# Kernel tuning notes

Hardware: AMD Instinct MI355X
Metric: run time of the kernel (lower is better)

Reference implementation:

```python
import jax, jax.numpy as jnp
import numpy as np

EMB = 1024
HEADS = 16
HD = EMB // HEADS  # 64
FF = 4 * EMB
EPS = 1e-5


def _layernorm(x, g, b):
    mu = jnp.mean(x, axis=-1, keepdims=True)
    var = jnp.mean(jnp.square(x - mu), axis=-1, keepdims=True)
    return (x - mu) * jax.lax.rsqrt(var + EPS) * g + b


def setup_inputs() -> dict:
    key = jax.random.key(0)
    ks = jax.random.split(key, 12)
    s_in = 1.0 / np.sqrt(EMB)
    s_ff = 1.0 / np.sqrt(FF)
    return {
        "x": jax.random.normal(ks[0], (4, 2048, EMB), dtype=jnp.float32),
        # per-head projections stacked: [H, C, HD]
        "Wq": jax.random.normal(ks[1], (HEADS, EMB, HD), dtype=jnp.float32) * s_in,
        "Wk": jax.random.normal(ks[2], (HEADS, EMB, HD), dtype=jnp.float32) * s_in,
        "Wv": jax.random.normal(ks[3], (HEADS, EMB, HD), dtype=jnp.float32) * s_in,
        "Wo": jax.random.normal(ks[4], (EMB, EMB), dtype=jnp.float32) * s_in,
        "bo": jnp.zeros((EMB,), dtype=jnp.float32),
        "W1": jax.random.normal(ks[5], (EMB, FF), dtype=jnp.float32) * s_in,
        "b1": jnp.zeros((FF,), dtype=jnp.float32),
        "W2": jax.random.normal(ks[6], (FF, EMB), dtype=jnp.float32) * s_ff,
        "b2": jnp.zeros((EMB,), dtype=jnp.float32),
        "g1": jnp.ones((EMB,), dtype=jnp.float32),
        "be1": jnp.zeros((EMB,), dtype=jnp.float32),
        "g2": jnp.ones((EMB,), dtype=jnp.float32),
        "be2": jnp.zeros((EMB,), dtype=jnp.float32),
    }


def reference(x, Wq, Wk, Wv, Wo, bo, W1, b1, W2, b2, g1, be1, g2, be2):
    B, T, C = x.shape
    h = _layernorm(x, g1, be1)
    # per-head projections: [B,H,T,HD]
    q = jnp.einsum("btc,hcd->bhtd", h, Wq)
    k = jnp.einsum("btc,hcd->bhtd", h, Wk)
    v = jnp.einsum("btc,hcd->bhtd", h, Wv)
    scores = jnp.einsum("bhtd,bhsd->bhts", q, k) * (HD ** -0.5)
    causal = jnp.tril(jnp.ones((T, T), dtype=bool))
    scores = jnp.where(causal, scores, -jnp.inf)
    attn = jax.nn.softmax(scores, axis=-1)
    out = jnp.einsum("bhts,bhsd->bhtd", attn, v)
    out = out.transpose(0, 2, 1, 3).reshape(B, T, C)  # concat heads
    x = x + out @ Wo + bo
    h2 = _layernorm(x, g2, be2)
    x = x + jax.nn.relu(h2 @ W1 + b1) @ W2 + b2
    return x
```

## Files before the change

### kernel.cpp

```cpp
#include <hip/hip_runtime.h>

typedef unsigned short u16;
typedef unsigned int u32;
typedef float f32x4 __attribute__((ext_vector_type(4)));
typedef short s16x8 __attribute__((ext_vector_type(8)));
typedef u16 u16x4 __attribute__((ext_vector_type(4)));
typedef u32 u32x2 __attribute__((ext_vector_type(2)));
typedef u32 u32x4 __attribute__((ext_vector_type(4)));

#define DEVI static __device__ __forceinline__

DEVI u16 f2bf(float f) {
  u32 u = __float_as_uint(f);
  return (u16)((u + 0x7fffu + ((u >> 16) & 1u)) >> 16);
}

DEVI float fexp2(float x) {
#if __has_builtin(__builtin_amdgcn_exp2f)
  return __builtin_amdgcn_exp2f(x);
#else
  return __expf(x * 0.69314718056f);
#endif
}

DEVI void g2l16(const void* g, void* l) {
  __builtin_amdgcn_global_load_lds((const __attribute__((address_space(1))) u32*)g,
                                   (__attribute__((address_space(3))) u32*)l,
                                   16, 0, 0);
}

__global__ __launch_bounds__(256) void trans_w(
    const float* __restrict__ src, u16* __restrict__ dst, int R, int C)
{
  __shared__ __attribute__((aligned(16))) u16 tile[64 * 65];
  const int t = threadIdx.x;
  const int c0 = blockIdx.x * 64, r0 = blockIdx.y * 64;
#pragma unroll
  for (int i = 0; i < 16; ++i) {
    const int idx = i * 256 + t;
    const int c = idx & 63, r = idx >> 6;
    tile[c * 65 + r] = f2bf(src[(long)(r0 + r) * C + c0 + c]);
  }
  __syncthreads();
#pragma unroll
  for (int i = 0; i < 16; ++i) {
    const int idx = i * 256 + t;
    const int r = idx & 63, c = idx >> 6;
    dst[(long)(c0 + c) * R + r0 + r] = tile[c * 65 + r];
  }
}

__global__ __launch_bounds__(256) void trans_qkvw(
    const float* __restrict__ Wq, const float* __restrict__ Wk,
    const float* __restrict__ Wv, u16* __restrict__ dst)
{
  __shared__ __attribute__((aligned(16))) u16 tile[64 * 65];
  const int t = threadIdx.x;
  const int c0 = blockIdx.x * 64;
  const int mh = blockIdx.y;
  const int mat = mh >> 4, h = mh & 15;
  const float* src = (mat == 0 ? Wq : (mat == 1 ? Wk : Wv)) + (long)h * 65536;
#pragma unroll
  for (int i = 0; i < 16; ++i) {
    const int idx = i * 256 + t;
    const int d = idx & 63, c = idx >> 6;
    tile[d * 65 + c] = f2bf(src[(long)(c0 + c) * 64 + d]);
  }
  __syncthreads();
  const long nb = (long)(mat * 1024 + h * 64);
#pragma unroll
  for (int i = 0; i < 16; ++i) {
    const int idx = i * 256 + t;
    const int d = idx >> 6, c = idx & 63;
    dst[(nb + d) * 1024 + c0 + c] = tile[d * 65 + c];
  }
}

__global__ __launch_bounds__(256) void vtrans(
    const u16* __restrict__ qkv, u16* __restrict__ vtg)
{
  __shared__ __attribute__((aligned(16))) u32 tile[64 * 33];
  const int t = threadIdx.x;
  const int tt = blockIdx.x, bh = blockIdx.y;
  const long bt0 = (long)(bh >> 4) * 2048;
  const int h = bh & 15;
  const int t0 = tt * 64;
  const int r2 = t >> 3, c8 = t & 7;
  const u16* src = qkv + (bt0 + t0 + 2 * r2) * 3072 + 2048 + h * 64 + c8 * 8;
  const s16x8 a = *(const s16x8*)src;
  const s16x8 b = *(const s16x8*)(src + 3072);
#pragma unroll
  for (int j = 0; j < 8; ++j)
    tile[(c8 * 8 + j) * 33 + r2] = (u32)(u16)a[j] | ((u32)(u16)b[j] << 16);
  __syncthreads();
#pragma unroll
  for (int it = 0; it < 2; ++it) {
    const int idx = it * 256 + t;
    const int d = idx >> 3, g = idx & 7;
    u32 p0 = tile[d * 33 + g];
    u32 p1 = tile[d * 33 + g + 8];
    u32 p2 = tile[d * 33 + g + 16];
    u32 p3 = tile[d * 33 + g + 24];
    u32x4 w;
    w[0] = (p0 & 0xffffu) | (p1 << 16);
    w[1] = (p2 & 0xffffu) | (p3 << 16);
    w[2] = (p0 >> 16) | (p1 & 0xffff0000u);
    w[3] = (p2 >> 16) | (p3 & 0xffff0000u);
    *(u32x4*)(vtg + (long)bh * 131072 + (long)d * 2048 + t0 + g * 8) = w;
  }
}

__global__ __launch_bounds__(256) void ln_kernel(
    const float* __restrict__ x, const float* __restrict__ g,
    const float* __restrict__ be, u16* __restrict__ out)
{
  const int t = threadIdx.x, wv = t >> 6, l = t & 63;
  const long row = (long)blockIdx.x * 4 + wv;
  const float* xr = x + row * 1024;
  f32x4 v[4];
#pragma unroll
  for (int i = 0; i < 4; ++i) v[i] = *(const f32x4*)(xr + i * 256 + l * 4);
  float s = 0.f, sq = 0.f;
#pragma unroll
  for (int i = 0; i < 4; ++i)
#pragma unroll
    for (int j = 0; j < 4; ++j) { s += v[i][j]; sq += v[i][j] * v[i][j]; }
#pragma unroll
  for (int mask = 1; mask < 64; mask <<= 1) {
    s  += __shfl_xor(s, mask);
    sq += __shfl_xor(sq, mask);
  }
  const float mean = s * (1.f / 1024.f);
  const float var  = sq * (1.f / 1024.f) - mean * mean;
  const float rs = rsqrtf(var + 1e-5f);
#pragma unroll
  for (int i = 0; i < 4; ++i) {
    f32x4 gv = *(const f32x4*)(g  + i * 256 + l * 4);
    f32x4 bv = *(const f32x4*)(be + i * 256 + l * 4);
    u16x4 o;
#pragma unroll
    for (int j = 0; j < 4; ++j) o[j] = f2bf((v[i][j] - mean) * rs * gv[j] + bv[j]);
    *(u16x4*)(out + row * 1024 + i * 256 + l * 4) = o;
  }
}

template <typename OutT, bool RELU, bool BIAS, bool RESID>
__global__ __launch_bounds__(256) void gemm_bt(
    const u16* __restrict__ A, const u16* __restrict__ Bt,
    OutT* __restrict__ Cout, const float* __restrict__ bias,
    const float* __restrict__ resid, int M, int N, int K)
{
  __shared__ __attribute__((aligned(16))) u16 As[4096];
  __shared__ __attribute__((aligned(16))) u16 Bs[4096];
  const int t  = threadIdx.x;
  const int l  = t & 63;
  const int wv = t >> 6;
  const int lr = l & 15, lg = l >> 4;
  const int wr = wv >> 1, wc = wv & 1;
  const long m0 = (long)blockIdx.x * 128, n0 = (long)blockIdx.y * 128;

  const int srow = t >> 2;
  const int scol = (t & 3) << 3;

  f32x4 acc[4][4] = {};

  const u16* Ap = A  + (m0 + srow) * K + scol;
  const u16* Bp = Bt + (n0 + srow) * K + scol;
  char* Asd = (char*)As + t * 16;
  char* Bsd = (char*)Bs + t * 16;

  for (int k0 = 0; k0 < K; k0 += 32) {
    __syncthreads();
    g2l16(Ap + k0,                Asd);
    g2l16(Ap + (long)64 * K + k0, Asd + 4096);
    g2l16(Bp + k0,                Bsd);
    g2l16(Bp + (long)64 * K + k0, Bsd + 4096);
    __syncthreads();
    s16x8 af[4], bfr[4];
#pragma unroll
    for (int m = 0; m < 4; ++m)
      af[m] = *(const s16x8*)(As + (wr * 64 + m * 16 + lr) * 32 + lg * 8);
#pragma unroll
    for (int n = 0; n < 4; ++n)
      bfr[n] = *(const s16x8*)(Bs + (wc * 64 + n * 16 + lr) * 32 + lg * 8);
#pragma unroll
    for (int m = 0; m < 4; ++m)
#pragma unroll
      for (int n = 0; n < 4; ++n)
        acc[m][n] = __builtin_amdgcn_mfma_f32_16x16x32_bf16(af[m], bfr[n], acc[m][n], 0, 0, 0);
  }

  float bv[4];
#pragma unroll
  for (int n = 0; n < 4; ++n)
    bv[n] = BIAS ? bias[n0 + wc * 64 + n * 16 + lr] : 0.f;

#pragma unroll
  for (int m = 0; m < 4; ++m) {
#pragma unroll
    for (int i = 0; i < 4; ++i) {
      const long row = m0 + wr * 64 + m * 16 + lg * 4 + i;
#pragma unroll
      for (int n = 0; n < 4; ++n) {
        const long col = n0 + wc * 64 + n * 16 + lr;
        float v = acc[m][n][i] + bv[n];
        if (RESID) v += resid[row * N + col];
        if (RELU)  v = fmaxf(v, 0.f);
        if constexpr (sizeof(OutT) == 2) Cout[row * N + col] = f2bf(v);
        else                             Cout[row * N + col] = v;
      }
    }
  }
}

__global__ __launch_bounds__(256) void attn_kernel(
    const u16* __restrict__ qkv, const u16* __restrict__ vtg,
    u16* __restrict__ out)
{
  __shared__ __attribute__((aligned(16))) u16 Kl[4096];
  __shared__ __attribute__((aligned(16))) u16 Vl[4096];
  __shared__ __attribute__((aligned(16))) u16 Pl[4][1024];

  const float c2 = 0.18033688011112042f;

  const int t  = threadIdx.x;
  const int wv = t >> 6, l = t & 63;
  const int lr = l & 15, lg = l >> 4;
  const int bh = blockIdx.y;
  const long bt0 = (long)(bh >> 4) * 2048;
  const int h = bh & 15;

  const int r0 = t >> 3, c8 = t & 7;
  const int swc = (c8 ^ (r0 & 7)) << 3;
  const u16* ksrc = qkv + (bt0 + r0) * 3072 + 1024 + h * 64 + swc;
  const u16* vsrc = vtg + (long)bh * 131072 + (long)r0 * 2048 + swc;
  char* kd = (char*)Kl + t * 16;
  char* vd = (char*)Vl + t * 16;
  char* pw = (char*)Pl + wv * 2048;

#pragma unroll
  for (int half = 0; half < 2; ++half) {
    const int qte = half ? (31 - (int)blockIdx.x) : (int)blockIdx.x;
    const int qrow0 = qte * 64 + wv * 16;

    s16x8 aq[2];
#pragma unroll
    for (int dc = 0; dc < 2; ++dc)
      aq[dc] = *(const s16x8*)(qkv + (bt0 + qrow0 + lr) * 3072 + h * 64 + dc * 32 + lg * 8);

    f32x4 O[4] = {};
    float mi[4], li[4];
#pragma unroll
    for (int i = 0; i < 4; ++i) { mi[i] = -__builtin_inff(); li[i] = 0.f; }

    for (int scn = 0; scn <= qte; ++scn) {
      const int s0 = scn * 64;
      __syncthreads();
      g2l16(ksrc + (long)s0 * 3072,        kd);
      g2l16(ksrc + (long)(s0 + 32) * 3072, kd + 4096);
      g2l16(vsrc + s0,                     vd);
      g2l16(vsrc + s0 + 65536,             vd + 4096);
      __syncthreads();

      s16x8 kf[4][2];
#pragma unroll
      for (int n = 0; n < 4; ++n) {
        const int row = n * 16 + lr;
        const int sw = (row & 7) << 4;
#pragma unroll
        for (int dh = 0; dh < 2; ++dh)
          kf[n][dh] = *(const s16x8*)((const char*)Kl + row * 128 +
                                      (((dh * 4 + lg) << 4) ^ sw));
      }

      f32x4 S[4];
#pragma unroll
      for (int n = 0; n < 4; ++n) {
        f32x4 z = {};
        z = __builtin_amdgcn_mfma_f32_16x16x32_bf16(aq[0], kf[n][0], z, 0, 0, 0);
        S[n] = __builtin_amdgcn_mfma_f32_16x16x32_bf16(aq[1], kf[n][1], z, 0, 0, 0);
      }

      float mt[4];
      if (scn == qte) {
#pragma unroll
        for (int i = 0; i < 4; ++i) {
          const int qg = qrow0 + lg * 4 + i;
#pragma unroll
          for (int n = 0; n < 4; ++n)
            S[n][i] = (s0 + n * 16 + lr <= qg) ? S[n][i] : -__builtin_inff();
          mt[i] = fmaxf(fmaxf(S[0][i], S[1][i]), fmaxf(S[2][i], S[3][i]));
        }
      } else {
#pragma unroll
        for (int i = 0; i < 4; ++i)
          mt[i] = fmaxf(fmaxf(S[0][i], S[1][i]), fmaxf(S[2][i], S[3][i]));
      }
#pragma unroll
      for (int msk = 1; msk < 16; msk <<= 1)
#pragma unroll
        for (int i = 0; i < 4; ++i)
          mt[i] = fmaxf(mt[i], __shfl_xor(mt[i], msk));

      const int grow = (mt[0] > mi[0]) | (mt[1] > mi[1]) |
                       (mt[2] > mi[2]) | (mt[3] > mi[3]);
      if (__any(grow)) {
#pragma unroll
        for (int i = 0; i < 4; ++i) {
          const float mn = fmaxf(mi[i], mt[i]);
          const float so = fexp2((mi[i] - mn) * c2);
          mi[i] = mn;
          li[i] *= so;
#pragma unroll
          for (int n = 0; n < 4; ++n) O[n][i] *= so;
        }
      }

#pragma unroll
      for (int i = 0; i < 4; ++i) {
        const float nmc = -mi[i] * c2;
        float p[4];
#pragma unroll
        for (int n = 0; n < 4; ++n) p[n] = fexp2(fmaf(S[n][i], c2, nmc));
        li[i] += (p[0] + p[1]) + (p[2] + p[3]);
        const int q_l = lg * 4 + i;
        u32x2 pk;
        pk[0] = (u32)f2bf(p[0]) | ((u32)f2bf(p[1]) << 16);
        pk[1] = (u32)f2bf(p[2]) | ((u32)f2bf(p[3]) << 16);
        *(u32x2*)(pw + q_l * 128 + ((((lr >> 1) << 4) ^ ((q_l & 7) << 4)) + ((lr & 1) << 3))) = pk;
      }

      s16x8 vf[4][2];
#pragma unroll
      for (int dn = 0; dn < 4; ++dn) {
        const int row = dn * 16 + lr;
        const int sw = (row & 7) << 4;
#pragma unroll
        for (int kk = 0; kk < 2; ++kk)
          vf[dn][kk] = *(const s16x8*)((const char*)Vl + row * 128 +
                                       (((kk * 4 + lg) << 4) ^ sw));
      }
      s16x8 pa[2];
#pragma unroll
      for (int kk = 0; kk < 2; ++kk)
        pa[kk] = *(const s16x8*)(pw + lr * 128 + (((kk * 4 + lg) << 4) ^ ((lr & 7) << 4)));
#pragma unroll
      for (int dn = 0; dn < 4; ++dn) {
        O[dn] = __builtin_amdgcn_mfma_f32_16x16x32_bf16(pa[0], vf[dn][0], O[dn], 0, 0, 0);
        O[dn] = __builtin_amdgcn_mfma_f32_16x16x32_bf16(pa[1], vf[dn][1], O[dn], 0, 0, 0);
      }
    }

#pragma unroll
    for (int msk = 1; msk < 16; msk <<= 1)
#pragma unroll
      for (int i = 0; i < 4; ++i)
        li[i] += __shfl_xor(li[i], msk);

#pragma unroll
    for (int i = 0; i < 4; ++i) {
      const float rl = 1.f / li[i];
      const long ob = (bt0 + qrow0 + lg * 4 + i) * 1024 + h * 64 + lr;
#pragma unroll
      for (int n = 0; n < 4; ++n)
        out[ob + n * 16] = f2bf(O[n][i] * rl);
    }
  }
}

extern "C" void kernel_launch(void* const* d_in, const int* in_sizes, int n_in,
                              void* d_out, int out_size, void* d_ws, size_t ws_size,
                              hipStream_t stream)
{
  const float* x   = (const float*)d_in[0];
  const float* Wq  = (const float*)d_in[1];
  const float* Wk  = (const float*)d_in[2];
  const float* Wv  = (const float*)d_in[3];
  const float* Wo  = (const float*)d_in[4];
  const float* bo  = (const float*)d_in[5];
  const float* W1  = (const float*)d_in[6];
  const float* b1  = (const float*)d_in[7];
  const float* W2  = (const float*)d_in[8];
  const float* b2  = (const float*)d_in[9];
  const float* g1  = (const float*)d_in[10];
  const float* be1 = (const float*)d_in[11];
  const float* g2  = (const float*)d_in[12];
  const float* be2 = (const float*)d_in[13];
  float* outp = (float*)d_out;

  char* ws = (char*)d_ws;
  u16*   qkvT = (u16*)ws;
  u16*   woT  = (u16*)(ws + 6291456);
  u16*   w1T  = (u16*)(ws + 8388608);
  u16*   w2T  = (u16*)(ws + 16777216);
  float* x2   = (float*)(ws + 25165824);
  u16*   attno= (u16*)(ws + 58720256);
  u16*   h2   = (u16*)(ws + 75497472);
  u16*   hbf  = (u16*)(ws + 92274688);
  u16*   vtg  = (u16*)(ws + 92274688);
  u16*   qkvb = (u16*)(ws + 109051904);
  u16*   ffn1 = (u16*)(ws + 92274688);
  (void)in_sizes; (void)n_in; (void)out_size; (void)ws_size;

  trans_qkvw<<<dim3(16, 48), 256, 0, stream>>>(Wq, Wk, Wv, qkvT);
  trans_w<<<dim3(16, 16), 256, 0, stream>>>(Wo, woT, 1024, 1024);
  trans_w<<<dim3(64, 16), 256, 0, stream>>>(W1, w1T, 1024, 4096);
  trans_w<<<dim3(16, 64), 256, 0, stream>>>(W2, w2T, 4096, 1024);

  ln_kernel<<<2048, 256, 0, stream>>>(x, g1, be1, hbf);
  gemm_bt<u16, false, false, false><<<dim3(64, 24), 256, 0, stream>>>(
      hbf, qkvT, qkvb, nullptr, nullptr, 8192, 3072, 1024);
  vtrans<<<dim3(32, 64), 256, 0, stream>>>(qkvb, vtg);
  attn_kernel<<<dim3(16, 64), 256, 0, stream>>>(qkvb, vtg, attno);
  gemm_bt<float, false, true, true><<<dim3(64, 8), 256, 0, stream>>>(
      attno, woT, x2, bo, x, 8192, 1024, 1024);
  ln_kernel<<<2048, 256, 0, stream>>>(x2, g2, be2, h2);
  gemm_bt<u16, true, true, false><<<dim3(64, 32), 256, 0, stream>>>(
      h2, w1T, ffn1, b1, nullptr, 8192, 4096, 1024);
  gemm_bt<float, false, true, true><<<dim3(64, 8), 256, 0, stream>>>(
      ffn1, w2T, outp, b2, x2, 8192, 1024, 4096);
}
```

Baseline: 551.8 us.

## Double-buffer GEMM LDS tiles with K=64 stages and XOR-swizzled layout

The bf16 GEMM mainloop now keeps two LDS buffers and prefetches the next K tile while MFMAs run on the current one. The K step grows from 32 to 64 and LDS rows are XOR-swizzled to avoid bank conflicts on fragment reads. This drops one barrier per iteration and hides global-to-LDS latency. The cost is four times the LDS (64 KB per block), which may lower occupancy.

```diff
diff --git a/kernel.cpp b/kernel.cpp
--- a/kernel.cpp
+++ b/kernel.cpp
@@ -150,8 +150,8 @@
     OutT* __restrict__ Cout, const float* __restrict__ bias,
     const float* __restrict__ resid, int M, int N, int K)
 {
-  __shared__ __attribute__((aligned(16))) u16 As[4096];
-  __shared__ __attribute__((aligned(16))) u16 Bs[4096];
+  __shared__ __attribute__((aligned(16))) u16 As[2][8192];
+  __shared__ __attribute__((aligned(16))) u16 Bs[2][8192];
   const int t  = threadIdx.x;
   const int l  = t & 63;
   const int wv = t >> 6;
@@ -159,36 +159,63 @@
   const int wr = wv >> 1, wc = wv & 1;
   const long m0 = (long)blockIdx.x * 128, n0 = (long)blockIdx.y * 128;
 
-  const int srow = t >> 2;
-  const int scol = (t & 3) << 3;
-
   f32x4 acc[4][4] = {};
 
-  const u16* Ap = A  + (m0 + srow) * K + scol;
-  const u16* Bp = Bt + (n0 + srow) * K + scol;
-  char* Asd = (char*)As + t * 16;
-  char* Bsd = (char*)Bs + t * 16;
-
-  for (int k0 = 0; k0 < K; k0 += 32) {
+  const int srow8 = t >> 3;
+  const int swc = ((t & 7) ^ (srow8 & 7)) << 3;
+  const u16* Ap = A  + (m0 + srow8) * K + swc;
+  const u16* Bp = Bt + (n0 + srow8) * K + swc;
+
+#define GSTAGE(buf, kof)                                                      \
+  {                                                                           \
+    _Pragma("unroll")                                                         \
+    for (int i = 0; i < 4; ++i) {                                             \
+      g2l16(Ap + (long)i * 32 * K + (kof), (char*)As[buf] + (i * 256 + t) * 16); \
+      g2l16(Bp + (long)i * 32 * K + (kof), (char*)Bs[buf] + (i * 256 + t) * 16); \
+    }                                                                         \
+  }
+
+#define GCOMPUTE(buf)                                                         \
+  {                                                                           \
+    const char* Ab = (const char*)As[buf];                                    \
+    const char* Bb = (const char*)Bs[buf];                                    \
+    _Pragma("unroll")                                                         \
+    for (int kk = 0; kk < 2; ++kk) {                                          \
+      s16x8 af[4], bfr[4];                                                    \
+      _Pragma("unroll")                                                       \
+      for (int m = 0; m < 4; ++m) {                                           \
+        const int row = wr * 64 + m * 16 + lr;                                \
+        af[m] = *(const s16x8*)(Ab + row * 128 +                              \
+                                ((((kk * 4 + lg) << 4) ^ ((row & 7) << 4)))); \
+      }                                                                       \
+      _Pragma("unroll")                                                       \
+      for (int n = 0; n < 4; ++n) {                                           \
+        const int row = wc * 64 + n * 16 + lr;                                \
+        bfr[n] = *(const s16x8*)(Bb + row * 128 +                             \
+                                 ((((kk * 4 + lg) << 4) ^ ((row & 7) << 4))));\
+      }                                                                       \
+      _Pragma("unroll")                                                       \
+      for (int m = 0; m < 4; ++m)                                             \
+        _Pragma("unroll")                                                     \
+        for (int n = 0; n < 4; ++n)                                           \
+          acc[m][n] = __builtin_amdgcn_mfma_f32_16x16x32_bf16(af[m], bfr[n],  \
+                                                              acc[m][n], 0, 0, 0); \
+    }                                                                         \
+  }
+
+  const int nt = K >> 6;
+  GSTAGE(0, 0);
+  __syncthreads();
+  int cur = 0;
+  for (int tt = 0; tt < nt - 1; ++tt) {
+    GSTAGE(cur ^ 1, (tt + 1) * 64);
+    GCOMPUTE(cur);
     __syncthreads();
-    g2l16(Ap + k0,                Asd);
-    g2l16(Ap + (long)64 * K + k0, Asd + 4096);
-    g2l16(Bp + k0,                Bsd);
-    g2l16(Bp + (long)64 * K + k0, Bsd + 4096);
-    __syncthreads();
-    s16x8 af[4], bfr[4];
-#pragma unroll
-    for (int m = 0; m < 4; ++m)
-      af[m] = *(const s16x8*)(As + (wr * 64 + m * 16 + lr) * 32 + lg * 8);
-#pragma unroll
-    for (int n = 0; n < 4; ++n)
-      bfr[n] = *(const s16x8*)(Bs + (wc * 64 + n * 16 + lr) * 32 + lg * 8);
-#pragma unroll
-    for (int m = 0; m < 4; ++m)
-#pragma unroll
-      for (int n = 0; n < 4; ++n)
-        acc[m][n] = __builtin_amdgcn_mfma_f32_16x16x32_bf16(af[m], bfr[n], acc[m][n], 0, 0, 0);
-  }
+    cur ^= 1;
+  }
+  GCOMPUTE(cur);
+#undef GSTAGE
+#undef GCOMPUTE
 
   float bv[4];
 #pragma unroll
```

Measured after the change: 517.1 us. -6.3%, faster.
